# Optimization experiments

Hardware: AMD Instinct MI355X
Metric: run time of the kernel (lower is better)

The kernel has to match this reference:

```python
import jax, jax.numpy as jnp
import numpy as np


def setup_inputs() -> dict:
    key = jax.random.key(0)
    k0, k1, k2, k3 = jax.random.split(key, 4)
    B, T, Din, H, Dout = 8, 4096, 1024, 1024, 1024
    x = jax.random.normal(k0, (B, T, Din), dtype=jnp.float32)
    # Linear weights stored torch-style as [out_features, in_features]
    W_hg = jax.random.normal(k1, (2 * H, Din), dtype=jnp.float32) * 0.02
    W_out = jax.random.normal(k2, (Dout, H), dtype=jnp.float32) * 0.02
    # episode-reset flags, 0/1 floats, shape [B,T,1] (expanded over channels)
    is_init = jax.random.bernoulli(k3, 0.01, (B, T, 1)).astype(jnp.float32)
    h_0 = jnp.zeros((B, 1, H), dtype=jnp.float32)
    return {"x": x, "W_hg": W_hg, "W_out": W_out, "is_init": is_init, "h_0": h_0}


def _mingru_scan(gate, hidden, is_init, h_0):
    # Linear recurrence h_t = (1-g_t) h_{t-1} + g_t * hidden_t, with resets.
    A = 1.0 - gate               # [B,T,H]
    Bv = gate * hidden           # [B,T,H]
    r = jnp.broadcast_to(is_init, Bv.shape)

    def combine(c1, c2):
        a1, b1, r1 = c1
        a2, b2, r2 = c2
        reset = r2 > 0
        a = jnp.where(reset, a2, a2 * a1)
        b = jnp.where(reset, b2, a2 * b1 + b2)
        return a, b, jnp.minimum(r1 + r2, 1.0)  # clamp(max=1)

    # Prepending the identity element then dropping it (as the torch code does)
    # is a no-op for an inclusive associative scan, so scan T elements directly.
    A_out, B_out, _ = jax.lax.associative_scan(combine, (A, Bv, r), axis=1)
    return A_out * h_0 + B_out   # h_0 is [B,1,H], broadcasts over T


def reference(x, W_hg, W_out, is_init, h_0):
    hg = jnp.einsum("btd,hd->bth", x, W_hg)          # [B,T,2H]
    hidden, gate = jnp.split(hg, 2, axis=-1)
    gate = jax.nn.sigmoid(gate)
    h = _mingru_scan(gate, hidden, is_init, h_0)      # [B,T,H]
    h_n = h[:, -1:]                                   # [B,1,H]
    out = jnp.einsum("bth,oh->bto", h, W_out)         # [B,T,Dout]
    return out, h_n
```

## Files before the change

### kernel.cpp

```cpp
#include <hip/hip_runtime.h>
#include <stdint.h>

#define B_DIM 8
#define T_DIM 4096
#define K_DIM 1024
#define H_DIM 1024
#define M_DIM (B_DIM * T_DIM)
#define CHUNK 64
#define NCHUNK (T_DIM / CHUNK)

typedef __attribute__((ext_vector_type(8))) short s16x8;
typedef __attribute__((ext_vector_type(4))) float f32x4;

__device__ __forceinline__ unsigned short f2b(float f) {
    union { float f; uint32_t u; } c; c.f = f;
    uint32_t r = (c.u + 0x7fffu + ((c.u >> 16) & 1u)) >> 16;
    return (unsigned short)r;
}
__device__ __forceinline__ float b2f(unsigned short u) {
    union { uint32_t u; float f; } c; c.u = ((uint32_t)u) << 16;
    return c.f;
}

__device__ __forceinline__ void gload_lds16(const unsigned short* g,
                                            unsigned short* l) {
    __builtin_amdgcn_global_load_lds(
        (__attribute__((address_space(1))) void*)g,
        (__attribute__((address_space(3))) void*)l, 16, 0, 0);
}

__device__ __forceinline__ void bar() {
    asm volatile("s_barrier" ::: "memory");
}


__global__ void cvt_f32_bf16(const float* __restrict__ src,
                             unsigned short* __restrict__ dst, int n4) {
    int stride = gridDim.x * blockDim.x;
    for (int i = blockIdx.x * blockDim.x + threadIdx.x; i < n4; i += stride) {
        float4 v = ((const float4*)src)[i];
        ushort4 o;
        o.x = f2b(v.x); o.y = f2b(v.y); o.z = f2b(v.z); o.w = f2b(v.w);
        ((ushort4*)dst)[i] = o;
    }
}

__global__ void prep_whg(const float* __restrict__ W,
                         unsigned short* __restrict__ Wp) {
    int i = blockIdx.x * blockDim.x + threadIdx.x;
    int total = 2 * H_DIM * K_DIM / 4;
    if (i >= total) return;
    int e = i * 4;
    int n = e >> 10;
    int k = e & 1023;
    int src = (n & 1) ? (H_DIM + (n >> 1)) : (n >> 1);
    float4 v = *(const float4*)&W[(size_t)src * K_DIM + k];
    ushort4 o;
    o.x = f2b(v.x); o.y = f2b(v.y); o.z = f2b(v.z); o.w = f2b(v.w);
    *(ushort4*)&Wp[(size_t)n * K_DIM + k] = o;
}


template <int EPI>
__global__ __launch_bounds__(512, 2) void gemm256(
    const unsigned short* __restrict__ A,
    const unsigned short* __restrict__ Bm,
    float* __restrict__ C,
    uint32_t* __restrict__ Sab,
    int N) {
    __shared__ unsigned short As[2][256 * 64];
    __shared__ unsigned short Bs[2][256 * 64];
    const int K = K_DIM;
    const int KT = K / 64;

    const int gx = gridDim.x;
    const int nwg = gx * gridDim.y;
    const int orig = blockIdx.y * gx + blockIdx.x;
    const int cpx = nwg >> 3;
    const int wg = (orig & 7) * cpx + (orig >> 3);
    const int m0 = (wg / gx) * 256;
    const int n0 = (wg % gx) * 256;

    const int t = threadIdx.x;
    const int lane = t & 63;
    const int w = t >> 6;
    const int wm = w >> 2, wn = w & 3;

    const int lrow = lane >> 3;
    const int lslot = (lane & 7) ^ lrow;

    const int l15 = lane & 15;
    const int rq = lane >> 4;
    const int rx = l15 & 7;

    f32x4 acc[8][4];
#pragma unroll
    for (int m = 0; m < 8; m++)
#pragma unroll
        for (int n = 0; n < 4; n++) acc[m][n] = (f32x4){0.f, 0.f, 0.f, 0.f};

    auto stageA = [&](int kt, int buf, int j) {
        const int seg = j * 8 + w;
        const int row = seg * 8 + lrow;
        gload_lds16(&A[(size_t)(m0 + row) * K + kt * 64 + lslot * 8],
                    &As[buf][seg * 512]);
    };
    auto stageB = [&](int kt, int buf, int j) {
        const int seg = j * 8 + w;
        const int row = seg * 8 + lrow;
        gload_lds16(&Bm[(size_t)(n0 + row) * K + kt * 64 + lslot * 8],
                    &Bs[buf][seg * 512]);
    };

    s16x8 af[4], bf[4];

#define LDA(buf, mi, ks) \
    (*(const s16x8*)&As[buf][(wm * 128 + (mi) * 16 + l15) * 64 + (((rq + (ks) * 4) ^ rx) * 8)])
#define LDB(buf, ni, ks) \
    (*(const s16x8*)&Bs[buf][(wn * 64 + (ni) * 16 + l15) * 64 + (((rq + (ks) * 4) ^ rx) * 8)])

#define MFMA16(MB)                                                          \
    __builtin_amdgcn_s_setprio(1);                                          \
    _Pragma("unroll") for (int m = 0; m < 4; m++)                           \
        _Pragma("unroll") for (int n = 0; n < 4; n++)                       \
            acc[MB + m][n] = __builtin_amdgcn_mfma_f32_16x16x32_bf16(       \
                af[m], bf[n], acc[MB + m][n], 0, 0, 0);                     \
    __builtin_amdgcn_s_setprio(0);

    {
#pragma unroll
        for (int j = 0; j < 4; j++) stageA(0, 0, j);
#pragma unroll
        for (int j = 0; j < 4; j++) stageB(0, 0, j);
        asm volatile("s_waitcnt vmcnt(0)" ::: "memory");
        bar();
    }

    for (int kt = 0; kt < KT; ++kt) {
        const int buf = kt & 1;
        const int nb = buf ^ 1;
        const bool nx = (kt + 1 < KT);
#pragma unroll
        for (int m = 0; m < 4; m++) af[m] = LDA(buf, m, 0);
#pragma unroll
        for (int n = 0; n < 4; n++) bf[n] = LDB(buf, n, 0);
        if (nx) { stageA(kt + 1, nb, 0); stageA(kt + 1, nb, 1); stageB(kt + 1, nb, 0); }
        bar();
        MFMA16(0);
        bar();
#pragma unroll
        for (int m = 0; m < 4; m++) af[m] = LDA(buf, m + 4, 0);
        if (nx) { stageA(kt + 1, nb, 2); stageA(kt + 1, nb, 3); stageB(kt + 1, nb, 1); }
        bar();
        MFMA16(4);
        bar();
#pragma unroll
        for (int m = 0; m < 4; m++) af[m] = LDA(buf, m, 1);
#pragma unroll
        for (int n = 0; n < 4; n++) bf[n] = LDB(buf, n, 1);
        if (nx) { stageB(kt + 1, nb, 2); stageB(kt + 1, nb, 3); }
        bar();
        MFMA16(0);
        bar();
#pragma unroll
        for (int m = 0; m < 4; m++) af[m] = LDA(buf, m + 4, 1);
        asm volatile("s_waitcnt vmcnt(0)" ::: "memory");
        bar();
        MFMA16(4);
        bar();
    }

    const int lr4 = rq * 4;
#pragma unroll
    for (int m = 0; m < 8; m++) {
#pragma unroll
        for (int n = 0; n < 4; n++) {
#pragma unroll
            for (int r = 0; r < 4; r++) {
                const int row = m0 + wm * 128 + m * 16 + lr4 + r;
                const int col = n0 + wn * 64 + n * 16 + l15;
                float v = acc[m][n][r];
                if (EPI == 0) {
                    C[(size_t)row * N + col] = v;
                } else {
                    float o = __shfl_xor(v, 1);
                    if ((lane & 1) == 0) {
                        float g = 1.f / (1.f + __expf(-o));
                        uint32_t pk = (uint32_t)f2b(1.f - g) |
                                      ((uint32_t)f2b(g * v) << 16);
                        Sab[(size_t)row * H_DIM + (col >> 1)] = pk;
                    }
                }
            }
        }
    }
#undef LDA
#undef LDB
#undef MFMA16
}


__global__ __launch_bounds__(256) void scan_chunks(
    const uint32_t* __restrict__ Sab, const float* __restrict__ is_init,
    float* __restrict__ CA, float* __restrict__ CB, float* __restrict__ CR) {
    int idx = blockIdx.x * 256 + threadIdx.x;
    int ch = idx & (H_DIM - 1);
    int chunk = (idx >> 10) & (NCHUNK - 1);
    int b = idx >> 16;
    int t0 = chunk * CHUNK;
    size_t base = ((size_t)b * T_DIM + t0) * H_DIM + ch;
    const float* ii = is_init + (size_t)b * T_DIM + t0;
    float A = 1.f, Bv = 0.f;
    int rf = 0;
    for (int i = 0; i < CHUNK; i++) {
        uint32_t d = Sab[base + (size_t)i * H_DIM];
        float a = b2f((unsigned short)(d & 0xffffu));
        float bb = b2f((unsigned short)(d >> 16));
        bool rst = ii[i] > 0.f;
        A = rst ? a : a * A;
        Bv = rst ? bb : fmaf(a, Bv, bb);
        rf |= (int)rst;
    }
    size_t o = ((size_t)b * NCHUNK + chunk) * H_DIM + ch;
    CA[o] = A;
    CB[o] = Bv;
    if (ch == 0) CR[b * NCHUNK + chunk] = (float)rf;
}

__global__ void scan_tops(const float* __restrict__ CA, const float* __restrict__ CB,
                          const float* __restrict__ CR,
                          float* __restrict__ PA, float* __restrict__ PB) {
    int idx = blockIdx.x * blockDim.x + threadIdx.x;
    if (idx >= B_DIM * H_DIM) return;
    int ch = idx & (H_DIM - 1);
    int b = idx >> 10;
    float A = 1.f, Bv = 0.f;
    for (int c = 0; c < NCHUNK; c++) {
        size_t o = ((size_t)b * NCHUNK + c) * H_DIM + ch;
        PA[o] = A;
        PB[o] = Bv;
        float a = CA[o], bb = CB[o];
        bool rst = CR[b * NCHUNK + c] > 0.f;
        float nA = rst ? a : a * A;
        float nB = rst ? bb : fmaf(a, Bv, bb);
        A = nA; Bv = nB;
    }
}

__global__ __launch_bounds__(256) void scan_apply(
    const uint32_t* __restrict__ Sab, const float* __restrict__ is_init,
    const float* __restrict__ PA, const float* __restrict__ PB,
    const float* __restrict__ h0,
    unsigned short* __restrict__ hb, float* __restrict__ hn) {
    int idx = blockIdx.x * 256 + threadIdx.x;
    int ch = idx & (H_DIM - 1);
    int chunk = (idx >> 10) & (NCHUNK - 1);
    int b = idx >> 16;
    int t0 = chunk * CHUNK;
    size_t base = ((size_t)b * T_DIM + t0) * H_DIM + ch;
    const float* ii = is_init + (size_t)b * T_DIM + t0;
    size_t po = ((size_t)b * NCHUNK + chunk) * H_DIM + ch;
    float A = PA[po], Bv = PB[po];
    float h0v = h0[b * H_DIM + ch];
    float h = 0.f;
    for (int i = 0; i < CHUNK; i++) {
        uint32_t d = Sab[base + (size_t)i * H_DIM];
        float a = b2f((unsigned short)(d & 0xffffu));
        float bb = b2f((unsigned short)(d >> 16));
        bool rst = ii[i] > 0.f;
        A = rst ? a : a * A;
        Bv = rst ? bb : fmaf(a, Bv, bb);
        h = fmaf(A, h0v, Bv);
        hb[base + (size_t)i * H_DIM] = f2b(h);
    }
    if (chunk == NCHUNK - 1) hn[b * H_DIM + ch] = h;
}


extern "C" void kernel_launch(void* const* d_in, const int* in_sizes, int n_in,
                              void* d_out, int out_size, void* d_ws, size_t ws_size,
                              hipStream_t stream) {
    const float* x       = (const float*)d_in[0];
    const float* W_hg    = (const float*)d_in[1];
    const float* W_out   = (const float*)d_in[2];
    const float* is_init = (const float*)d_in[3];
    const float* h0      = (const float*)d_in[4];
    float* out = (float*)d_out;
    float* hn  = out + (size_t)M_DIM * H_DIM;

    char* ws = (char*)d_ws;
    size_t off = 0;
    auto alloc = [&](size_t bytes) {
        void* p = ws + off;
        off += (bytes + 255) & ~(size_t)255;
        return p;
    };
    unsigned short* xb  = (unsigned short*)alloc((size_t)M_DIM * K_DIM * 2);
    unsigned short* Wp  = (unsigned short*)alloc((size_t)2 * H_DIM * K_DIM * 2);
    unsigned short* Wob = (unsigned short*)alloc((size_t)H_DIM * K_DIM * 2);
    uint32_t* Sab = (uint32_t*)alloc((size_t)M_DIM * H_DIM * 4);
    float* CA = (float*)alloc((size_t)B_DIM * NCHUNK * H_DIM * 4);
    float* CB = (float*)alloc((size_t)B_DIM * NCHUNK * H_DIM * 4);
    float* CR = (float*)alloc((size_t)B_DIM * NCHUNK * 4);
    float* PA = (float*)alloc((size_t)B_DIM * NCHUNK * H_DIM * 4);
    float* PB = (float*)alloc((size_t)B_DIM * NCHUNK * H_DIM * 4);
    unsigned short* hb = xb;

    cvt_f32_bf16<<<2048, 256, 0, stream>>>(x, xb, M_DIM * K_DIM / 4);
    prep_whg<<<(2 * H_DIM * K_DIM / 4 + 255) / 256, 256, 0, stream>>>(W_hg, Wp);
    cvt_f32_bf16<<<1024, 256, 0, stream>>>(W_out, Wob, H_DIM * K_DIM / 4);

    gemm256<1><<<dim3(2048 / 256, M_DIM / 256), 512, 0, stream>>>(
        xb, Wp, nullptr, Sab, 2048);

    scan_chunks<<<(B_DIM * NCHUNK * H_DIM) / 256, 256, 0, stream>>>(
        Sab, is_init, CA, CB, CR);
    scan_tops<<<(B_DIM * H_DIM + 255) / 256, 256, 0, stream>>>(CA, CB, CR, PA, PB);
    scan_apply<<<(B_DIM * NCHUNK * H_DIM) / 256, 256, 0, stream>>>(
        Sab, is_init, PA, PB, h0, hb, hn);

    gemm256<0><<<dim3(1024 / 256, M_DIM / 256), 512, 0, stream>>>(
        hb, Wob, out, nullptr, 1024);
}
```

Baseline: 354.6 us.

## Fuse chunk-level scan reduction into gate GEMM epilogue and merge conversion kernels

The first GEMM's epilogue now computes per-64-row chunk scan aggregates (A, B, reset flag) directly from the accumulator registers using in-register combines and cross-lane shuffles, removing the separate scan_chunks kernel that re-read the whole Sab buffer. The three fp32-to-bf16 conversion launches are merged into one grid-stride kernel. The aggregates are computed from fp32 values rather than the bf16-rounded ones stored in Sab, so they may differ slightly from what scan_apply later uses. The epilogue also gains extra register pressure and shuffles.

Result: slower. 503.5 us (+42.0%).

```diff
diff --git a/kernel.cpp b/kernel.cpp
--- a/kernel.cpp
+++ b/kernel.cpp
@@ -33,31 +33,56 @@
     asm volatile("s_barrier" ::: "memory");
 }
 
-
-__global__ void cvt_f32_bf16(const float* __restrict__ src,
-                             unsigned short* __restrict__ dst, int n4) {
-    int stride = gridDim.x * blockDim.x;
-    for (int i = blockIdx.x * blockDim.x + threadIdx.x; i < n4; i += stride) {
-        float4 v = ((const float4*)src)[i];
-        ushort4 o;
-        o.x = f2b(v.x); o.y = f2b(v.y); o.z = f2b(v.z); o.w = f2b(v.w);
-        ((ushort4*)dst)[i] = o;
-    }
-}
-
-__global__ void prep_whg(const float* __restrict__ W,
-                         unsigned short* __restrict__ Wp) {
-    int i = blockIdx.x * blockDim.x + threadIdx.x;
-    int total = 2 * H_DIM * K_DIM / 4;
-    if (i >= total) return;
-    int e = i * 4;
-    int n = e >> 10;
-    int k = e & 1023;
-    int src = (n & 1) ? (H_DIM + (n >> 1)) : (n >> 1);
-    float4 v = *(const float4*)&W[(size_t)src * K_DIM + k];
+struct Xf { float A, B; int R; };
+__device__ __forceinline__ Xf xcomb(Xf c1, Xf c2) {
+    Xf o;
+    o.A = c2.R ? c2.A : c2.A * c1.A;
+    o.B = c2.R ? c2.B : fmaf(c2.A, c1.B, c2.B);
+    o.R = c1.R | c2.R;
+    return o;
+}
+__device__ __forceinline__ Xf xshfl(Xf s, int src) {
+    Xf o;
+    o.A = __shfl(s.A, src);
+    o.B = __shfl(s.B, src);
+    o.R = __shfl(s.R, src);
+    return o;
+}
+
+
+__device__ __forceinline__ ushort4 cvu4(float4 v) {
     ushort4 o;
     o.x = f2b(v.x); o.y = f2b(v.y); o.z = f2b(v.z); o.w = f2b(v.w);
-    *(ushort4*)&Wp[(size_t)n * K_DIM + k] = o;
+    return o;
+}
+
+__global__ void cvt_all(const float* __restrict__ x,
+                        const float* __restrict__ Whg,
+                        const float* __restrict__ Wout,
+                        unsigned short* __restrict__ xb,
+                        unsigned short* __restrict__ Wp,
+                        unsigned short* __restrict__ Wob) {
+    const int NX = M_DIM * K_DIM / 4;
+    const int NW = 2 * H_DIM * K_DIM / 4;
+    const int NO = H_DIM * K_DIM / 4;
+    int stride = gridDim.x * blockDim.x;
+    for (int i = blockIdx.x * blockDim.x + threadIdx.x; i < NX + NW + NO;
+         i += stride) {
+        if (i < NX) {
+            ((ushort4*)xb)[i] = cvu4(((const float4*)x)[i]);
+        } else if (i < NX + NW) {
+            int j = i - NX;
+            int e = j * 4;
+            int n = e >> 10;
+            int k = e & 1023;
+            int src = (n & 1) ? (H_DIM + (n >> 1)) : (n >> 1);
+            *(ushort4*)&Wp[(size_t)n * K_DIM + k] =
+                cvu4(*(const float4*)&Whg[(size_t)src * K_DIM + k]);
+        } else {
+            int j = i - NX - NW;
+            ((ushort4*)Wob)[j] = cvu4(((const float4*)Wout)[j]);
+        }
+    }
 }
 
 
@@ -67,6 +92,8 @@
     const unsigned short* __restrict__ Bm,
     float* __restrict__ C,
     uint32_t* __restrict__ Sab,
+    const float* __restrict__ II,
+    float* __restrict__ CA, float* __restrict__ CB, float* __restrict__ CR,
     int N) {
     __shared__ unsigned short As[2][256 * 64];
     __shared__ unsigned short Bs[2][256 * 64];
@@ -170,28 +197,79 @@
         bar();
     }
 
-    const int lr4 = rq * 4;
-#pragma unroll
-    for (int m = 0; m < 8; m++) {
+    if (EPI == 0) {
+#pragma unroll
+        for (int m = 0; m < 8; m++)
+#pragma unroll
+            for (int n = 0; n < 4; n++)
+#pragma unroll
+                for (int r = 0; r < 4; r++) {
+                    const int row = m0 + wm * 128 + m * 16 + rq * 4 + r;
+                    const int col = n0 + wn * 64 + n * 16 + l15;
+                    C[(size_t)row * N + col] = acc[m][n][r];
+                }
+    } else {
+        float* ldsI = (float*)As;
+        if (t < 256) ldsI[t] = II[m0 + t];
+        __syncthreads();
+        uint32_t rmask = 0;
+#pragma unroll
+        for (int m = 0; m < 8; m++) {
+            float4 rv = *(const float4*)&ldsI[wm * 128 + m * 16 + rq * 4];
+            rmask |= (rv.x > 0.f ? 1u : 0u) << (m * 4 + 0);
+            rmask |= (rv.y > 0.f ? 1u : 0u) << (m * 4 + 1);
+            rmask |= (rv.z > 0.f ? 1u : 0u) << (m * 4 + 2);
+            rmask |= (rv.w > 0.f ? 1u : 0u) << (m * 4 + 3);
+        }
+        Xf cLo[4], cHi[4];
 #pragma unroll
         for (int n = 0; n < 4; n++) {
-#pragma unroll
-            for (int r = 0; r < 4; r++) {
-                const int row = m0 + wm * 128 + m * 16 + lr4 + r;
-                const int col = n0 + wn * 64 + n * 16 + l15;
-                float v = acc[m][n][r];
-                if (EPI == 0) {
-                    C[(size_t)row * N + col] = v;
-                } else {
+            cLo[n] = (Xf){1.f, 0.f, 0};
+            cHi[n] = (Xf){1.f, 0.f, 0};
+        }
+#pragma unroll
+        for (int m = 0; m < 8; m++) {
+#pragma unroll
+            for (int n = 0; n < 4; n++) {
+                Xf seg = (Xf){1.f, 0.f, 0};
+#pragma unroll
+                for (int r = 0; r < 4; r++) {
+                    const int row = m0 + wm * 128 + m * 16 + rq * 4 + r;
+                    const int col = n0 + wn * 64 + n * 16 + l15;
+                    float v = acc[m][n][r];
                     float o = __shfl_xor(v, 1);
+                    float g = 1.f / (1.f + __expf(-o));
+                    float a = 1.f - g;
+                    float bb = g * v;
                     if ((lane & 1) == 0) {
-                        float g = 1.f / (1.f + __expf(-o));
-                        uint32_t pk = (uint32_t)f2b(1.f - g) |
-                                      ((uint32_t)f2b(g * v) << 16);
+                        uint32_t pk = (uint32_t)f2b(a) |
+                                      ((uint32_t)f2b(bb) << 16);
                         Sab[(size_t)row * H_DIM + (col >> 1)] = pk;
                     }
+                    Xf e = (Xf){a, bb, (int)((rmask >> (m * 4 + r)) & 1u)};
+                    seg = xcomb(seg, e);
                 }
+                Xf c = xshfl(seg, l15);
+#pragma unroll
+                for (int q = 1; q < 4; q++) c = xcomb(c, xshfl(seg, q * 16 + l15));
+                if (m < 4) cLo[n] = xcomb(cLo[n], c);
+                else       cHi[n] = xcomb(cHi[n], c);
             }
+        }
+        const int bcLo = (m0 + wm * 128) >> 6;
+        if ((lane & 1) == 0 && rq == 0) {
+#pragma unroll
+            for (int n = 0; n < 4; n++) {
+                const int ch = (n0 + wn * 64 + n * 16 + l15) >> 1;
+                CA[(size_t)bcLo * H_DIM + ch] = cLo[n].A;
+                CB[(size_t)bcLo * H_DIM + ch] = cLo[n].B;
+                CA[(size_t)(bcLo + 1) * H_DIM + ch] = cHi[n].A;
+                CB[(size_t)(bcLo + 1) * H_DIM + ch] = cHi[n].B;
+            }
+        }
+        if (lane == 0 && wn == 0) {
+            CR[bcLo] = (float)cLo[0].R;
+            CR[bcLo + 1] = (float)cHi[0].R;
         }
     }
 #undef LDA
@@ -199,33 +277,6 @@
 #undef MFMA16
 }
 
-
-__global__ __launch_bounds__(256) void scan_chunks(
-    const uint32_t* __restrict__ Sab, const float* __restrict__ is_init,
-    float* __restrict__ CA, float* __restrict__ CB, float* __restrict__ CR) {
-    int idx = blockIdx.x * 256 + threadIdx.x;
-    int ch = idx & (H_DIM - 1);
-    int chunk = (idx >> 10) & (NCHUNK - 1);
-    int b = idx >> 16;
-    int t0 = chunk * CHUNK;
-    size_t base = ((size_t)b * T_DIM + t0) * H_DIM + ch;
-    const float* ii = is_init + (size_t)b * T_DIM + t0;
-    float A = 1.f, Bv = 0.f;
-    int rf = 0;
-    for (int i = 0; i < CHUNK; i++) {
-        uint32_t d = Sab[base + (size_t)i * H_DIM];
-        float a = b2f((unsigned short)(d & 0xffffu));
-        float bb = b2f((unsigned short)(d >> 16));
-        bool rst = ii[i] > 0.f;
-        A = rst ? a : a * A;
-        Bv = rst ? bb : fmaf(a, Bv, bb);
-        rf |= (int)rst;
-    }
-    size_t o = ((size_t)b * NCHUNK + chunk) * H_DIM + ch;
-    CA[o] = A;
-    CB[o] = Bv;
-    if (ch == 0) CR[b * NCHUNK + chunk] = (float)rf;
-}
 
 __global__ void scan_tops(const float* __restrict__ CA, const float* __restrict__ CB,
                           const float* __restrict__ CR,
@@ -306,19 +357,15 @@
     float* PB = (float*)alloc((size_t)B_DIM * NCHUNK * H_DIM * 4);
     unsigned short* hb = xb;
 
-    cvt_f32_bf16<<<2048, 256, 0, stream>>>(x, xb, M_DIM * K_DIM / 4);
-    prep_whg<<<(2 * H_DIM * K_DIM / 4 + 255) / 256, 256, 0, stream>>>(W_hg, Wp);
-    cvt_f32_bf16<<<1024, 256, 0, stream>>>(W_out, Wob, H_DIM * K_DIM / 4);
+    cvt_all<<<2048, 256, 0, stream>>>(x, W_hg, W_out, xb, Wp, Wob);
 
     gemm256<1><<<dim3(2048 / 256, M_DIM / 256), 512, 0, stream>>>(
-        xb, Wp, nullptr, Sab, 2048);
-
-    scan_chunks<<<(B_DIM * NCHUNK * H_DIM) / 256, 256, 0, stream>>>(
-        Sab, is_init, CA, CB, CR);
+        xb, Wp, nullptr, Sab, is_init, CA, CB, CR, 2048);
+
     scan_tops<<<(B_DIM * H_DIM + 255) / 256, 256, 0, stream>>>(CA, CB, CR, PA, PB);
     scan_apply<<<(B_DIM * NCHUNK * H_DIM) / 256, 256, 0, stream>>>(
         Sab, is_init, PA, PB, h0, hb, hn);
 
     gemm256<0><<<dim3(1024 / 256, M_DIM / 256), 512, 0, stream>>>(
-        hb, Wob, out, nullptr, 1024);
-}
+        hb, Wob, out, nullptr, nullptr, nullptr, nullptr, nullptr, 1024);
+}
```
